# Performance work log

Measured on AMD Instinct MI355X. Metric: run time of the kernel, lower is better.

## Reference

```python
import jax, jax.numpy as jnp
import numpy as np

N = 100000      # nodes
E = 3200000     # edges (before self-loops)
F_IN = 1433
H1, D1 = 8, 8   # layer1: 8 heads, 8 dims each -> concat 64
H2, D2 = 1, 7   # layer2: 1 head, 7 classes
NEG_SLOPE = 0.2


def setup_inputs() -> dict:
    key = jax.random.key(0)
    ks = jax.random.split(key, 10)
    x = jax.random.normal(ks[0], (N, F_IN), dtype=jnp.float32)
    edge_index = jax.random.randint(ks[1], (2, E), 0, N, dtype=jnp.int32)
    W1 = jax.random.normal(ks[2], (F_IN, H1 * D1), dtype=jnp.float32) * np.float32(1.0 / np.sqrt(F_IN))
    a1_src = jax.random.normal(ks[3], (H1, D1), dtype=jnp.float32) * 0.1
    a1_dst = jax.random.normal(ks[4], (H1, D1), dtype=jnp.float32) * 0.1
    b1 = jnp.zeros((H1 * D1,), dtype=jnp.float32)
    W2 = jax.random.normal(ks[5], (H1 * D1, H2 * D2), dtype=jnp.float32) * np.float32(1.0 / np.sqrt(H1 * D1))
    a2_src = jax.random.normal(ks[6], (H2, D2), dtype=jnp.float32) * 0.1
    a2_dst = jax.random.normal(ks[7], (H2, D2), dtype=jnp.float32) * 0.1
    b2 = jnp.zeros((D2,), dtype=jnp.float32)
    return {"x": x, "edge_index": edge_index, "W1": W1, "a1_src": a1_src,
            "a1_dst": a1_dst, "b1": b1, "W2": W2, "a2_src": a2_src,
            "a2_dst": a2_dst, "b2": b2}


def gat_layer(x, src, dst, W, a_s, a_d, b, concat):
    n = x.shape[0]
    H, D = a_s.shape
    h = (x @ W).reshape(n, H, D)                       # [N, H, D] projected features
    alpha_s = jnp.einsum('nhd,hd->nh', h, a_s)         # [N, H]
    alpha_d = jnp.einsum('nhd,hd->nh', h, a_d)
    e = jax.nn.leaky_relu(alpha_s[src] + alpha_d[dst], NEG_SLOPE)  # [E, H]
    # scatter-softmax over edges grouped by destination node
    m = jax.ops.segment_max(e, dst, num_segments=n)
    e = jnp.exp(e - m[dst])
    s = jax.ops.segment_sum(e, dst, num_segments=n)
    alpha = e / (s[dst] + 1e-16)                       # [E, H]
    msg = h[src] * alpha[:, :, None]                   # [E, H, D]
    out = jax.ops.segment_sum(msg, dst, num_segments=n)  # [N, H, D]
    out = out.reshape(n, H * D) if concat else out.mean(axis=1)
    return out + b


def reference(x, edge_index, W1, a1_src, a1_dst, b1, W2, a2_src, a2_dst, b2):
    n = x.shape[0]
    loops = jnp.arange(n, dtype=edge_index.dtype)
    src = jnp.concatenate([edge_index[0], loops])      # add self-loops (PyG default)
    dst = jnp.concatenate([edge_index[1], loops])
    h = jax.nn.relu(gat_layer(x, src, dst, W1, a1_src, a1_dst, b1, concat=True))
    # F.dropout is a no-op in eval mode
    h = gat_layer(h, src, dst, W2, a2_src, a2_dst, b2, concat=False)
    return jax.nn.log_softmax(h, axis=1)
```

## Files before the change

### kernel.cpp

```cpp
#include <hip/hip_runtime.h>

#define NN 100000
#define FIN 1433
#define KSTEPS 45
#define CAP 96
#define NBIN 391
#define BCAP 8704

typedef __attribute__((ext_vector_type(8))) short s16x8;
typedef __attribute__((ext_vector_type(4))) float f32x4;

__device__ __forceinline__ short f2bf(float f){
  unsigned u = __float_as_uint(f);
  unsigned r = (u + 0x7fffu + ((u >> 16) & 1u)) >> 16;
  return (short)r;
}
__device__ __forceinline__ float bflo(unsigned u){ return __uint_as_float(u << 16); }
__device__ __forceinline__ float bfhi(unsigned u){ return __uint_as_float(u & 0xffff0000u); }

__device__ __forceinline__ f32x4 mfma16(s16x8 a, s16x8 b, f32x4 c){
  return __builtin_amdgcn_mfma_f32_16x16x32_bf16(a, b, c, 0, 0, 0);
}

__global__ void w1pack_k(const float* __restrict__ W1, short* __restrict__ pack){
  int unit = blockIdx.x * 4 + (threadIdx.x >> 6);
  if (unit < KSTEPS * 4){
    int ks = unit >> 2, nf = unit & 3, l = threadIdx.x & 63;
    int col = nf * 16 + (l & 15);
    s16x8 v;
    #pragma unroll
    for (int j = 0; j < 8; j++){
      int k = ks * 32 + ((l >> 4) * 8) + j;
      float f = (k < FIN) ? W1[k * 64 + col] : 0.0f;
      v[j] = f2bf(f);
    }
    *(s16x8*)&pack[((size_t)unit * 64 + l) * 8] = v;
  }
}

__global__ void pass1_k(const int* __restrict__ srcs, const int* __restrict__ dsts,
                        int* __restrict__ cursor, uint2* __restrict__ ebuf, int E8){
  __shared__ int cntB[NBIN];
  __shared__ int baseB[NBIN];
  int t = threadIdx.x;
  for (int j = t; j < NBIN; j += 256) cntB[j] = 0;
  __syncthreads();
  int i = blockIdx.x * 256 + t;
  int sv[8], dv[8], rk[8];
  bool act = i < E8;
  if (act){
    int4 s0 = ((const int4*)srcs)[2 * i], s1 = ((const int4*)srcs)[2 * i + 1];
    int4 d0 = ((const int4*)dsts)[2 * i], d1 = ((const int4*)dsts)[2 * i + 1];
    sv[0]=s0.x; sv[1]=s0.y; sv[2]=s0.z; sv[3]=s0.w;
    sv[4]=s1.x; sv[5]=s1.y; sv[6]=s1.z; sv[7]=s1.w;
    dv[0]=d0.x; dv[1]=d0.y; dv[2]=d0.z; dv[3]=d0.w;
    dv[4]=d1.x; dv[5]=d1.y; dv[6]=d1.z; dv[7]=d1.w;
    #pragma unroll
    for (int j = 0; j < 8; j++) rk[j] = atomicAdd(&cntB[dv[j] >> 8], 1);
  }
  __syncthreads();
  for (int j = t; j < NBIN; j += 256){
    int c = cntB[j];
    baseB[j] = c ? atomicAdd(&cursor[j], c) : 0;
  }
  __syncthreads();
  if (act){
    #pragma unroll
    for (int j = 0; j < 8; j++){
      int bin = dv[j] >> 8;
      int pos = baseB[bin] + rk[j];
      if (pos < BCAP) ebuf[(size_t)bin * BCAP + pos] = make_uint2((unsigned)sv[j], (unsigned)dv[j]);
    }
  }
}

__global__ __launch_bounds__(256, 4) void k2_k(const float* __restrict__ x,
                                               const short* __restrict__ w1p,
                                               unsigned short* __restrict__ h1b,
                                               const float* __restrict__ a1s,
                                               const float* __restrict__ a1d,
                                               float* __restrict__ as1,
                                               float* __restrict__ ad1,
                                               int n, int Ggemm,
                                               const int* __restrict__ cursor,
                                               const uint2* __restrict__ ebuf,
                                               int* __restrict__ cnt,
                                               int* __restrict__ colv){
  __shared__ float lds[4][2][16][36];
  __shared__ int lcnt[256];
  if (blockIdx.x < NBIN){
    int bin = blockIdx.x;
    int t = threadIdx.x;
    int n0 = bin << 8;
    int node = n0 + t;
    bool valid = node < n;
    lcnt[t] = 1;
    if (valid) colv[(size_t)node * CAP] = node;
    __syncthreads();
    int ec = min(cursor[bin], BCAP);
    const uint2* eb = ebuf + (size_t)bin * BCAP;
    for (int i = t; i < ec; i += 256){
      uint2 e = eb[i];
      int p = atomicAdd(&lcnt[(int)e.y - n0], 1);
      if (p < CAP) colv[(size_t)e.y * CAP + p] = (int)e.x;
    }
    __syncthreads();
    if (valid) cnt[node] = lcnt[t];
    return;
  }
  int gb = blockIdx.x - NBIN;
  if (gb >= Ggemm) return;
  int tid = threadIdx.x;
  int wid = tid >> 6, lane = tid & 63;
  int row0 = gb * 64 + wid * 16;
  f32x4 acc[4] = {};

  int lr = lane >> 5, lc = lane & 31;
  const float* pj[8];
  #pragma unroll
  for (int j = 0; j < 8; j++){
    int rg = min(row0 + j * 2 + lr, n - 1);
    pj[j] = x + (size_t)rg * FIN + lc;
  }
  int frow = lane & 15, fg = lane >> 4;
  const s16x8* pb = ((const s16x8*)w1p) + lane;

  float r[8];
  #pragma unroll
  for (int j = 0; j < 8; j++) r[j] = pj[j][0];

#define STAGE_COMPUTE(KS, RBUF)                                           \
  {                                                                       \
    float (&buf)[16][36] = lds[wid][(KS) & 1];                            \
    _Pragma("unroll")                                                     \
    for (int j = 0; j < 8; j++) buf[j * 2 + lr][lc] = RBUF[j];            \
    f32x4 lo = *(const f32x4*)&buf[frow][fg * 8];                         \
    f32x4 hi = *(const f32x4*)&buf[frow][fg * 8 + 4];                     \
    s16x8 a0;                                                             \
    _Pragma("unroll")                                                     \
    for (int j = 0; j < 4; j++){ a0[j] = f2bf(lo[j]); a0[j+4] = f2bf(hi[j]); } \
    s16x8 b0 = pb[((KS) * 4 + 0) * 64];                                   \
    s16x8 b1 = pb[((KS) * 4 + 1) * 64];                                   \
    s16x8 b2 = pb[((KS) * 4 + 2) * 64];                                   \
    s16x8 b3 = pb[((KS) * 4 + 3) * 64];                                   \
    acc[0] = mfma16(a0, b0, acc[0]);                                      \
    acc[1] = mfma16(a0, b1, acc[1]);                                      \
    acc[2] = mfma16(a0, b2, acc[2]);                                      \
    acc[3] = mfma16(a0, b3, acc[3]);                                      \
  }

  #pragma unroll 2
  for (int ks = 0; ks < 44; ks++){
    float r2[8];
    if (ks == 43){
      int toff = (lc < 25) ? 44 * 32 : 0;
      #pragma unroll
      for (int j = 0; j < 8; j++){
        float v = pj[j][toff];
        r2[j] = (lc < 25) ? v : 0.0f;
      }
    } else {
      int off = (ks + 1) * 32;
      #pragma unroll
      for (int j = 0; j < 8; j++) r2[j] = pj[j][off];
    }
    STAGE_COMPUTE(ks, r);
    #pragma unroll
    for (int j = 0; j < 8; j++) r[j] = r2[j];
  }
  STAGE_COMPUTE(44, r);
#undef STAGE_COMPUTE

  #pragma unroll
  for (int r4 = 0; r4 < 4; r4++){
    int m = row0 + (lane >> 4) * 4 + r4;
    if (m < n){
      #pragma unroll
      for (int nf = 0; nf < 4; nf++){
        float v = acc[nf][r4];
        float pv = __shfl_xor(v, 1);
        if ((lane & 1) == 0){
          unsigned pk = (unsigned)(unsigned short)f2bf(v) |
                        ((unsigned)(unsigned short)f2bf(pv) << 16);
          *(unsigned*)&h1b[(size_t)m * 64 + nf * 16 + (lane & 15)] = pk;
        }
      }
    }
  }

  int p = lane & 15;
  float cs[4], cd[4];
  #pragma unroll
  for (int nf = 0; nf < 4; nf++){
    cs[nf] = a1s[nf * 16 + p];
    cd[nf] = a1d[nf * 16 + p];
  }
  int b = (lane >> 3) & 1;
  #pragma unroll
  for (int r4 = 0; r4 < 4; r4++){
    int m = row0 + (lane >> 4) * 4 + r4;
    float s[4], d[4];
    #pragma unroll
    for (int nf = 0; nf < 4; nf++){
      s[nf] = acc[nf][r4] * cs[nf];
      d[nf] = acc[nf][r4] * cd[nf];
      s[nf] += __shfl_xor(s[nf], 1); d[nf] += __shfl_xor(d[nf], 1);
      s[nf] += __shfl_xor(s[nf], 2); d[nf] += __shfl_xor(d[nf], 2);
      s[nf] += __shfl_xor(s[nf], 4); d[nf] += __shfl_xor(d[nf], 4);
    }
    if ((lane & 7) == 0 && m < n){
      #pragma unroll
      for (int nf = 0; nf < 4; nf++){
        as1[m * 8 + 2 * nf + b] = s[nf];
        ad1[m * 8 + 2 * nf + b] = d[nf];
      }
    }
  }
}

__global__ void agg1_k(const int* __restrict__ cnt, const int* __restrict__ colv,
                       const unsigned short* __restrict__ h1b,
                       const float* __restrict__ as1, const float* __restrict__ ad1,
                       const float* __restrict__ b1, const float* __restrict__ W2,
                       const float* __restrict__ a2s, const float* __restrict__ a2d,
                       float* __restrict__ h2, float* __restrict__ vs2,
                       float* __restrict__ vd2, int n){
  int node = blockIdx.x * 4 + (threadIdx.x >> 6);
  if (node >= n) return;
  int l = threadIdx.x & 63, sl = l & 7, qw = l >> 3;
  float adn = ad1[node * 8 + sl];
  float a[8] = {0,0,0,0,0,0,0,0};
  float sw = 0.0f;
  int beg = node * CAP, end = beg + min(cnt[node], CAP);
  for (int i = beg + qw; i < end; i += 8){
    int s0 = colv[i];
    float e0 = as1[s0 * 8 + sl] + adn;
    uint4 u = *(const uint4*)(h1b + (size_t)s0 * 64 + 8 * sl);
    e0 = e0 > 0.0f ? e0 : 0.2f * e0;
    float w0 = __expf(e0);
    a[0] += w0 * bflo(u.x); a[1] += w0 * bfhi(u.x);
    a[2] += w0 * bflo(u.y); a[3] += w0 * bfhi(u.y);
    a[4] += w0 * bflo(u.z); a[5] += w0 * bfhi(u.z);
    a[6] += w0 * bflo(u.w); a[7] += w0 * bfhi(u.w);
    sw += w0;
  }
  sw += __shfl_xor(sw, 8); sw += __shfl_xor(sw, 16); sw += __shfl_xor(sw, 32);
  #pragma unroll
  for (int j = 0; j < 8; j++){
    a[j] += __shfl_xor(a[j], 8);
    a[j] += __shfl_xor(a[j], 16);
    a[j] += __shfl_xor(a[j], 32);
  }

  float inv = 1.0f / (sw + 1e-16f);
  float4 bv0 = *(const float4*)&b1[8 * sl];
  float4 bv1 = *(const float4*)&b1[8 * sl + 4];
  float o[8];
  o[0] = a[0] * inv + bv0.x; o[1] = a[1] * inv + bv0.y;
  o[2] = a[2] * inv + bv0.z; o[3] = a[3] * inv + bv0.w;
  o[4] = a[4] * inv + bv1.x; o[5] = a[5] * inv + bv1.y;
  o[6] = a[6] * inv + bv1.z; o[7] = a[7] * inv + bv1.w;
  #pragma unroll
  for (int j = 0; j < 8; j++) o[j] = o[j] > 0.0f ? o[j] : 0.0f;

  const float* wr = W2 + 56 * sl;
  float dot[7];
  #pragma unroll
  for (int c = 0; c < 7; c++){
    float s = 0.0f;
    #pragma unroll
    for (int j = 0; j < 8; j++) s += o[j] * wr[7 * j + c];
    dot[c] = s;
  }
  #pragma unroll
  for (int c = 0; c < 7; c++){
    dot[c] += __shfl_xor(dot[c], 1);
    dot[c] += __shfl_xor(dot[c], 2);
    dot[c] += __shfl_xor(dot[c], 4);
  }
  if (l < 7) h2[(size_t)node * 7 + l] = dot[l];
  if (l == 0){
    float s = 0.0f, d = 0.0f;
    #pragma unroll
    for (int c = 0; c < 7; c++){
      s += dot[c] * a2s[c];
      d += dot[c] * a2d[c];
    }
    vs2[node] = s; vd2[node] = d;
  }
}

__global__ void agg2_k(const int* __restrict__ cnt, const int* __restrict__ colv,
                       const float* __restrict__ h2, const float* __restrict__ vs2,
                       const float* __restrict__ vd2, const float* __restrict__ b2,
                       float* __restrict__ out, int n){
  int node = blockIdx.x * 4 + (threadIdx.x >> 6);
  if (node >= n) return;
  int l = threadIdx.x & 63, c = l & 7, qw = l >> 3;
  bool cls = c < 7;
  float adn = vd2[node];
  float acc = 0.0f, sw = 0.0f;
  int beg = node * CAP, end = beg + min(cnt[node], CAP);
  int i = beg + qw;
  for (; i + 8 < end; i += 16){
    int s0 = colv[i], s1 = colv[i + 8];
    float e0 = vs2[s0] + adn;
    float e1 = vs2[s1] + adn;
    float v0 = cls ? h2[(size_t)s0 * 7 + c] : 0.0f;
    float v1 = cls ? h2[(size_t)s1 * 7 + c] : 0.0f;
    e0 = e0 > 0.0f ? e0 : 0.2f * e0;
    e1 = e1 > 0.0f ? e1 : 0.2f * e1;
    float w0 = __expf(e0), w1 = __expf(e1);
    acc += w0 * v0 + w1 * v1;
    sw += w0 + w1;
  }
  if (i < end){
    int s0 = colv[i];
    float e0 = vs2[s0] + adn;
    e0 = e0 > 0.0f ? e0 : 0.2f * e0;
    float w0 = __expf(e0);
    acc += w0 * (cls ? h2[(size_t)s0 * 7 + c] : 0.0f);
    sw += w0;
  }
  acc += __shfl_xor(acc, 8);  acc += __shfl_xor(acc, 16); acc += __shfl_xor(acc, 32);
  sw  += __shfl_xor(sw, 8);   sw  += __shfl_xor(sw, 16);  sw  += __shfl_xor(sw, 32);
  if (qw == 0){
    float inv = 1.0f / (sw + 1e-16f);
    float o = cls ? acc * inv + b2[c] : -1e30f;
    float m = o;
    m = fmaxf(m, __shfl_xor(m, 1, 8));
    m = fmaxf(m, __shfl_xor(m, 2, 8));
    m = fmaxf(m, __shfl_xor(m, 4, 8));
    float ex = cls ? __expf(o - m) : 0.0f;
    float s8 = ex;
    s8 += __shfl_xor(s8, 1, 8);
    s8 += __shfl_xor(s8, 2, 8);
    s8 += __shfl_xor(s8, 4, 8);
    if (cls) out[(size_t)node * 7 + c] = o - m - __logf(s8);
  }
}

extern "C" void kernel_launch(void* const* d_in, const int* in_sizes, int n_in,
                              void* d_out, int out_size, void* d_ws, size_t ws_size,
                              hipStream_t stream){
  const float* x   = (const float*)d_in[0];
  const int*   ei  = (const int*)d_in[1];
  const float* W1  = (const float*)d_in[2];
  const float* a1s = (const float*)d_in[3];
  const float* a1d = (const float*)d_in[4];
  const float* b1  = (const float*)d_in[5];
  const float* W2  = (const float*)d_in[6];
  const float* a2s = (const float*)d_in[7];
  const float* a2d = (const float*)d_in[8];
  const float* b2  = (const float*)d_in[9];
  int E = in_sizes[1] / 2;
  const int* srcs = ei;
  const int* dsts = ei + E;
  int n = in_sizes[0] / FIN;

  char* ws = (char*)d_ws;
  size_t off = 0;
  auto alloc = [&](size_t bytes)->void*{
    void* p = ws + off; off += (bytes + 255) & ~(size_t)255; return p;
  };
  unsigned short* h1b = (unsigned short*)alloc((size_t)n * 64 * 2);
  float* as1  = (float*)alloc((size_t)n * 8 * 4);
  float* ad1  = (float*)alloc((size_t)n * 8 * 4);
  float* h2   = (float*)alloc((size_t)n * 7 * 4);
  float* vs2  = (float*)alloc((size_t)n * 4);
  float* vd2  = (float*)alloc((size_t)n * 4);
  int* cnt    = (int*)alloc((size_t)(n + 256) * 4);
  int* colv   = (int*)alloc((size_t)n * CAP * 4);
  short* w1p  = (short*)alloc((size_t)KSTEPS * 4 * 64 * 8 * 2);
  uint2* ebuf = (uint2*)alloc((size_t)NBIN * BCAP * 8);
  int* cursor = (int*)alloc((size_t)NBIN * 4);
  (void)ws_size; (void)n_in; (void)out_size;

  int E8 = E / 8;
  int Gp1 = (E8 + 255) / 256;
  int Ggemm = (n + 63) / 64;

  hipMemsetAsync(cursor, 0, (size_t)NBIN * 4, stream);
  w1pack_k<<<(KSTEPS * 4 + 3) / 4, 256, 0, stream>>>(W1, w1p);
  pass1_k<<<Gp1, 256, 0, stream>>>(srcs, dsts, cursor, ebuf, E8);
  k2_k<<<NBIN + Ggemm, 256, 0, stream>>>(x, w1p, h1b, a1s, a1d, as1, ad1,
                                         n, Ggemm, cursor, ebuf, cnt, colv);
  agg1_k<<<(n + 3) / 4, 256, 0, stream>>>(cnt, colv, h1b, as1, ad1, b1,
                                          W2, a2s, a2d, h2, vs2, vd2, n);
  agg2_k<<<(n + 3) / 4, 256, 0, stream>>>(cnt, colv, h2, vs2, vd2, b2,
                                          (float*)d_out, n);
}
```

Before: 479.0 us.

## Coarsen edge binning per block, fold cursor reset into pack kernel, raise occupancy

The edge-binning pass now has each block process eight chunks of edges. It counts per-bin totals first, reserves global space once per bin, then re-reads the edges and scatters them using LDS atomic slot counters, so far fewer global atomics are issued on the cursor array. The memset of the cursor array is folded into an extra block of the W1 packing kernel, which removes one launch. The GEMM/binning kernel's launch bounds are raised to 8 blocks per CU, which may force register spills. Edges are read twice and the order of edges within a bin becomes nondeterministic.

After: 491.6 us. 2.6% more time.

```diff
diff --git a/kernel.cpp b/kernel.cpp
--- a/kernel.cpp
+++ b/kernel.cpp
@@ -6,6 +6,7 @@
 #define CAP 96
 #define NBIN 391
 #define BCAP 8704
+#define P1C 8
 
 typedef __attribute__((ext_vector_type(8))) short s16x8;
 typedef __attribute__((ext_vector_type(4))) float f32x4;
@@ -22,7 +23,12 @@
   return __builtin_amdgcn_mfma_f32_16x16x32_bf16(a, b, c, 0, 0, 0);
 }
 
-__global__ void w1pack_k(const float* __restrict__ W1, short* __restrict__ pack){
+__global__ void w1pack_k(const float* __restrict__ W1, short* __restrict__ pack,
+                         int* __restrict__ cursor){
+  if (blockIdx.x == 45){
+    for (int j = threadIdx.x; j < NBIN; j += 256) cursor[j] = 0;
+    return;
+  }
   int unit = blockIdx.x * 4 + (threadIdx.x >> 6);
   if (unit < KSTEPS * 4){
     int ks = unit >> 2, nf = unit & 3, l = threadIdx.x & 63;
@@ -41,40 +47,47 @@
 __global__ void pass1_k(const int* __restrict__ srcs, const int* __restrict__ dsts,
                         int* __restrict__ cursor, uint2* __restrict__ ebuf, int E8){
   __shared__ int cntB[NBIN];
-  __shared__ int baseB[NBIN];
+  __shared__ int wcnt[NBIN];
   int t = threadIdx.x;
   for (int j = t; j < NBIN; j += 256) cntB[j] = 0;
   __syncthreads();
-  int i = blockIdx.x * 256 + t;
-  int sv[8], dv[8], rk[8];
-  bool act = i < E8;
-  if (act){
-    int4 s0 = ((const int4*)srcs)[2 * i], s1 = ((const int4*)srcs)[2 * i + 1];
-    int4 d0 = ((const int4*)dsts)[2 * i], d1 = ((const int4*)dsts)[2 * i + 1];
-    sv[0]=s0.x; sv[1]=s0.y; sv[2]=s0.z; sv[3]=s0.w;
-    sv[4]=s1.x; sv[5]=s1.y; sv[6]=s1.z; sv[7]=s1.w;
-    dv[0]=d0.x; dv[1]=d0.y; dv[2]=d0.z; dv[3]=d0.w;
-    dv[4]=d1.x; dv[5]=d1.y; dv[6]=d1.z; dv[7]=d1.w;
-    #pragma unroll
-    for (int j = 0; j < 8; j++) rk[j] = atomicAdd(&cntB[dv[j] >> 8], 1);
+  int base = blockIdx.x * (256 * P1C);
+  for (int c = 0; c < P1C; c++){
+    int i = base + c * 256 + t;
+    if (i < E8){
+      int4 d0 = ((const int4*)dsts)[2 * i], d1 = ((const int4*)dsts)[2 * i + 1];
+      atomicAdd(&cntB[d0.x >> 8], 1);
+      atomicAdd(&cntB[d0.y >> 8], 1);
+      atomicAdd(&cntB[d0.z >> 8], 1);
+      atomicAdd(&cntB[d0.w >> 8], 1);
+      atomicAdd(&cntB[d1.x >> 8], 1);
+      atomicAdd(&cntB[d1.y >> 8], 1);
+      atomicAdd(&cntB[d1.z >> 8], 1);
+      atomicAdd(&cntB[d1.w >> 8], 1);
+    }
   }
   __syncthreads();
-  for (int j = t; j < NBIN; j += 256){
-    int c = cntB[j];
-    baseB[j] = c ? atomicAdd(&cursor[j], c) : 0;
-  }
+  for (int j = t; j < NBIN; j += 256)
+    wcnt[j] = cntB[j] ? atomicAdd(&cursor[j], cntB[j]) : 0;
   __syncthreads();
-  if (act){
-    #pragma unroll
-    for (int j = 0; j < 8; j++){
-      int bin = dv[j] >> 8;
-      int pos = baseB[bin] + rk[j];
-      if (pos < BCAP) ebuf[(size_t)bin * BCAP + pos] = make_uint2((unsigned)sv[j], (unsigned)dv[j]);
-    }
-  }
-}
-
-__global__ __launch_bounds__(256, 4) void k2_k(const float* __restrict__ x,
+  for (int c = 0; c < P1C; c++){
+    int i = base + c * 256 + t;
+    if (i < E8){
+      int4 s0 = ((const int4*)srcs)[2 * i], s1 = ((const int4*)srcs)[2 * i + 1];
+      int4 d0 = ((const int4*)dsts)[2 * i], d1 = ((const int4*)dsts)[2 * i + 1];
+      int sv[8] = {s0.x, s0.y, s0.z, s0.w, s1.x, s1.y, s1.z, s1.w};
+      int dv[8] = {d0.x, d0.y, d0.z, d0.w, d1.x, d1.y, d1.z, d1.w};
+      #pragma unroll
+      for (int j = 0; j < 8; j++){
+        int bin = dv[j] >> 8;
+        int p = atomicAdd(&wcnt[bin], 1);
+        if (p < BCAP) ebuf[(size_t)bin * BCAP + p] = make_uint2((unsigned)sv[j], (unsigned)dv[j]);
+      }
+    }
+  }
+}
+
+__global__ __launch_bounds__(256, 8) void k2_k(const float* __restrict__ x,
                                                const short* __restrict__ w1p,
                                                unsigned short* __restrict__ h1b,
                                                const float* __restrict__ a1s,
@@ -377,11 +390,10 @@
   (void)ws_size; (void)n_in; (void)out_size;
 
   int E8 = E / 8;
-  int Gp1 = (E8 + 255) / 256;
+  int Gp1 = (E8 + 256 * P1C - 1) / (256 * P1C);
   int Ggemm = (n + 63) / 64;
 
-  hipMemsetAsync(cursor, 0, (size_t)NBIN * 4, stream);
-  w1pack_k<<<(KSTEPS * 4 + 3) / 4, 256, 0, stream>>>(W1, w1p);
+  w1pack_k<<<46, 256, 0, stream>>>(W1, w1p, cursor);
   pass1_k<<<Gp1, 256, 0, stream>>>(srcs, dsts, cursor, ebuf, E8);
   k2_k<<<NBIN + Ggemm, 256, 0, stream>>>(x, w1p, h1b, a1s, a1d, as1, ad1,
                                          n, Ggemm, cursor, ebuf, cnt, colv);
```

## Deepen GEMM prefetch pipeline, fold cursor memset into pack kernel, reorder blocks

Applied to the files above, without the earlier changes.

The x-projection GEMM loop now prefetches global rows two k-steps ahead instead of one. It writes the next stage into the LDS double buffer before the current stage is consumed, aiming to hide more global-load latency in this memory-bound stream over x. The cursor memset is folded into an extra block of the W1 pack kernel, which removes one API call. GEMM blocks are placed before the bin-bucketing blocks in k2 so the long GEMM work is dispatched first. The extra prefetch stage costs more registers at launch bounds (256,4).

Result: no change. 478.0 us (-0.2%).

```diff
diff --git a/kernel.cpp b/kernel.cpp
--- a/kernel.cpp
+++ b/kernel.cpp
@@ -22,7 +22,12 @@
   return __builtin_amdgcn_mfma_f32_16x16x32_bf16(a, b, c, 0, 0, 0);
 }
 
-__global__ void w1pack_k(const float* __restrict__ W1, short* __restrict__ pack){
+__global__ void w1pack_k(const float* __restrict__ W1, short* __restrict__ pack,
+                         int* __restrict__ cursor){
+  if (blockIdx.x == 45){
+    for (int j = threadIdx.x; j < NBIN; j += 256) cursor[j] = 0;
+    return;
+  }
   int unit = blockIdx.x * 4 + (threadIdx.x >> 6);
   if (unit < KSTEPS * 4){
     int ks = unit >> 2, nf = unit & 3, l = threadIdx.x & 63;
@@ -88,8 +93,8 @@
                                                int* __restrict__ colv){
   __shared__ float lds[4][2][16][36];
   __shared__ int lcnt[256];
-  if (blockIdx.x < NBIN){
-    int bin = blockIdx.x;
+  if (blockIdx.x >= Ggemm){
+    int bin = blockIdx.x - Ggemm;
     int t = threadIdx.x;
     int n0 = bin << 8;
     int node = n0 + t;
@@ -108,11 +113,9 @@
     if (valid) cnt[node] = lcnt[t];
     return;
   }
-  int gb = blockIdx.x - NBIN;
-  if (gb >= Ggemm) return;
   int tid = threadIdx.x;
   int wid = tid >> 6, lane = tid & 63;
-  int row0 = gb * 64 + wid * 16;
+  int row0 = blockIdx.x * 64 + wid * 16;
   f32x4 acc[4] = {};
 
   int lr = lane >> 5, lc = lane & 31;
@@ -125,51 +128,54 @@
   int frow = lane & 15, fg = lane >> 4;
   const s16x8* pb = ((const s16x8*)w1p) + lane;
 
-  float r[8];
-  #pragma unroll
-  for (int j = 0; j < 8; j++) r[j] = pj[j][0];
-
-#define STAGE_COMPUTE(KS, RBUF)                                           \
-  {                                                                       \
-    float (&buf)[16][36] = lds[wid][(KS) & 1];                            \
-    _Pragma("unroll")                                                     \
-    for (int j = 0; j < 8; j++) buf[j * 2 + lr][lc] = RBUF[j];            \
-    f32x4 lo = *(const f32x4*)&buf[frow][fg * 8];                         \
-    f32x4 hi = *(const f32x4*)&buf[frow][fg * 8 + 4];                     \
-    s16x8 a0;                                                             \
-    _Pragma("unroll")                                                     \
-    for (int j = 0; j < 4; j++){ a0[j] = f2bf(lo[j]); a0[j+4] = f2bf(hi[j]); } \
-    s16x8 b0 = pb[((KS) * 4 + 0) * 64];                                   \
-    s16x8 b1 = pb[((KS) * 4 + 1) * 64];                                   \
-    s16x8 b2 = pb[((KS) * 4 + 2) * 64];                                   \
-    s16x8 b3 = pb[((KS) * 4 + 3) * 64];                                   \
-    acc[0] = mfma16(a0, b0, acc[0]);                                      \
-    acc[1] = mfma16(a0, b1, acc[1]);                                      \
-    acc[2] = mfma16(a0, b2, acc[2]);                                      \
-    acc[3] = mfma16(a0, b3, acc[3]);                                      \
+  float rB[8], rC[8];
+  {
+    float rA[8];
+    #pragma unroll
+    for (int j = 0; j < 8; j++) rA[j] = pj[j][0];
+    #pragma unroll
+    for (int j = 0; j < 8; j++) rB[j] = pj[j][32];
+    float (&b0)[16][36] = lds[wid][0];
+    #pragma unroll
+    for (int j = 0; j < 8; j++) b0[j * 2 + lr][lc] = rA[j];
   }
 
   #pragma unroll 2
-  for (int ks = 0; ks < 44; ks++){
-    float r2[8];
-    if (ks == 43){
+  for (int ks = 0; ks <= 44; ks++){
+    int ld = ks + 2;
+    if (ld < 44){
+      #pragma unroll
+      for (int j = 0; j < 8; j++) rC[j] = pj[j][ld * 32];
+    } else if (ld == 44){
       int toff = (lc < 25) ? 44 * 32 : 0;
       #pragma unroll
       for (int j = 0; j < 8; j++){
         float v = pj[j][toff];
-        r2[j] = (lc < 25) ? v : 0.0f;
+        rC[j] = (lc < 25) ? v : 0.0f;
       }
-    } else {
-      int off = (ks + 1) * 32;
-      #pragma unroll
-      for (int j = 0; j < 8; j++) r2[j] = pj[j][off];
-    }
-    STAGE_COMPUTE(ks, r);
-    #pragma unroll
-    for (int j = 0; j < 8; j++) r[j] = r2[j];
-  }
-  STAGE_COMPUTE(44, r);
-#undef STAGE_COMPUTE
+    }
+    if (ks < 44){
+      float (&bufn)[16][36] = lds[wid][(ks + 1) & 1];
+      #pragma unroll
+      for (int j = 0; j < 8; j++) bufn[j * 2 + lr][lc] = rB[j];
+    }
+    float (&buf)[16][36] = lds[wid][ks & 1];
+    f32x4 lo = *(const f32x4*)&buf[frow][fg * 8];
+    f32x4 hi = *(const f32x4*)&buf[frow][fg * 8 + 4];
+    s16x8 a0;
+    #pragma unroll
+    for (int j = 0; j < 4; j++){ a0[j] = f2bf(lo[j]); a0[j + 4] = f2bf(hi[j]); }
+    s16x8 b0 = pb[(ks * 4 + 0) * 64];
+    s16x8 b1 = pb[(ks * 4 + 1) * 64];
+    s16x8 b2 = pb[(ks * 4 + 2) * 64];
+    s16x8 b3 = pb[(ks * 4 + 3) * 64];
+    acc[0] = mfma16(a0, b0, acc[0]);
+    acc[1] = mfma16(a0, b1, acc[1]);
+    acc[2] = mfma16(a0, b2, acc[2]);
+    acc[3] = mfma16(a0, b3, acc[3]);
+    #pragma unroll
+    for (int j = 0; j < 8; j++) rB[j] = rC[j];
+  }
 
   #pragma unroll
   for (int r4 = 0; r4 < 4; r4++){
@@ -380,10 +386,9 @@
   int Gp1 = (E8 + 255) / 256;
   int Ggemm = (n + 63) / 64;
 
-  hipMemsetAsync(cursor, 0, (size_t)NBIN * 4, stream);
-  w1pack_k<<<(KSTEPS * 4 + 3) / 4, 256, 0, stream>>>(W1, w1p);
+  w1pack_k<<<46, 256, 0, stream>>>(W1, w1p, cursor);
   pass1_k<<<Gp1, 256, 0, stream>>>(srcs, dsts, cursor, ebuf, E8);
-  k2_k<<<NBIN + Ggemm, 256, 0, stream>>>(x, w1p, h1b, a1s, a1d, as1, ad1,
+  k2_k<<<Ggemm + NBIN, 256, 0, stream>>>(x, w1p, h1b, a1s, a1d, as1, ad1,
                                          n, Ggemm, cursor, ebuf, cnt, colv);
   agg1_k<<<(n + 3) / 4, 256, 0, stream>>>(cnt, colv, h1b, as1, ad1, b1,
                                           W2, a2s, a2d, h2, vs2, vd2, n);
```
